# Kernel optimization log

Hardware: AMD Instinct MI355X
Metric: run time of the kernel (lower is better)

## Reference

```python
import jax, jax.numpy as jnp
import numpy as np
from jax import lax

B, T, V, E, H, C, K = 256, 512, 50000, 128, 256, 128, 2


def setup_inputs() -> dict:
    key = jax.random.key(0)
    ks = jax.random.split(key, 16)
    s = lambda *sh: 1.0 / np.sqrt(sh[0])
    return {
        "input_current": jax.random.randint(ks[0], (B, T), 0, V, dtype=jnp.int32),
        "input_left": jax.random.randint(ks[1], (B, T), 0, V, dtype=jnp.int32),
        "input_right": jax.random.randint(ks[2], (B, T), 0, V, dtype=jnp.int32),
        "emb": jax.random.normal(ks[3], (V, E), jnp.float32) * 0.05,
        "Wf": jax.random.normal(ks[4], (E, H), jnp.float32) * s(E),
        "Uf": jax.random.normal(ks[5], (H, H), jnp.float32) * s(H),
        "bf": jnp.zeros((H,), jnp.float32),
        "Wb": jax.random.normal(ks[6], (E, H), jnp.float32) * s(E),
        "Ub": jax.random.normal(ks[7], (H, H), jnp.float32) * s(H),
        "bb": jnp.zeros((H,), jnp.float32),
        "Wc": jax.random.normal(ks[8], (2 * H + E, C), jnp.float32) * s(2 * H + E),
        "bc": jnp.zeros((C,), jnp.float32),
        "Wd": jax.random.normal(ks[9], (C, K), jnp.float32) * s(C),
        "bd": jnp.zeros((K,), jnp.float32),
    }


def _simple_rnn(x, W, U, b):
    # x: [B,T,E] -> outputs [B,T,H]; h_t = tanh(x_t W + b + h_{t-1} U)
    xw = jnp.einsum("bte,eh->bth", x, W) + b  # precompute input projection
    h0 = jnp.zeros((x.shape[0], U.shape[0]), x.dtype)

    def step(h, xw_t):
        h = jnp.tanh(xw_t + h @ U)
        return h, h

    _, hs = lax.scan(step, h0, jnp.swapaxes(xw, 0, 1))  # scan over time
    return jnp.swapaxes(hs, 0, 1)


def reference(input_current, input_left, input_right, emb, Wf, Uf, bf, Wb, Ub, bb, Wc, bc, Wd, bd):
    e_cur = emb[input_current]  # [B,T,E]
    e_left = emb[input_left]
    e_right = emb[input_right]
    x_left = _simple_rnn(e_left, Wf, Uf, bf)  # [B,T,H]
    # go_backwards RNN: process reversed sequence, then model reverses back
    x_right = _simple_rnn(e_right[:, ::-1], Wb, Ub, bb)[:, ::-1]  # [B,T,H]
    x = jnp.concatenate([x_left, e_cur, x_right], axis=2)  # [B,T,2H+E]
    x = jnp.tanh(jnp.einsum("btd,dc->btc", x, Wc) + bc)  # Conv1D k=1 + tanh
    x = jnp.max(x, axis=1)  # GlobalMaxPooling1D
    return jax.nn.sigmoid(x @ Wd + bd)  # [B,K]
```

## Files before the change

### kernel.cpp

```cpp
#include <hip/hip_runtime.h>
#include <hip/hip_bf16.h>


#define B_ 256
#define T_ 512
#define E_ 128
#define H_ 256
#define C_ 128

typedef __attribute__((ext_vector_type(8))) short short8;
typedef __attribute__((ext_vector_type(4))) float float4v;
typedef __attribute__((ext_vector_type(2))) unsigned int uint2v;

__device__ inline unsigned short f2bf(float f) {
  unsigned u = __float_as_uint(f);
  u += 0x7fffu + ((u >> 16) & 1u);
  return (unsigned short)(u >> 16);
}
__device__ inline unsigned pkbf(float a, float b) {
  __hip_bfloat162 h2 = __float22bfloat162_rn(float2{a, b});
  union { __hip_bfloat162 h; unsigned u; } cv;
  cv.h = h2;
  return cv.u;
}
__device__ inline float lo16f(unsigned u) { return __uint_as_float(u << 16); }
__device__ inline float hi16f(unsigned u) { return __uint_as_float(u & 0xffff0000u); }
__device__ inline float fast_tanh(float x) {
  float e = __expf(2.f * x);
  float r = __builtin_amdgcn_rcpf(e + 1.f);
  return __builtin_fmaf(-2.f, r, 1.f);
}
__device__ inline unsigned enc_f(float f) {
  unsigned u = __float_as_uint(f);
  return (u & 0x80000000u) ? ~u : (u | 0x80000000u);
}
__device__ inline float dec_f(unsigned key) {
  unsigned bits = (key & 0x80000000u) ? (key ^ 0x80000000u) : ~key;
  return __uint_as_float(bits);
}
__device__ inline void sync_lds() {
  asm volatile("s_waitcnt lgkmcnt(0)\n\ts_barrier" ::: "memory");
}
__device__ inline int clampt(int t) { return t < 0 ? 0 : (t > 511 ? 511 : t); }

__device__ inline void wait_flag(const int* f) {
  if (__hip_atomic_load(f, __ATOMIC_RELAXED, __HIP_MEMORY_SCOPE_AGENT) == 0) {
    while (__hip_atomic_load(f, __ATOMIC_RELAXED, __HIP_MEMORY_SCOPE_AGENT) ==
           0)
      __builtin_amdgcn_s_sleep(8);
  }
  (void)__hip_atomic_load(f, __ATOMIC_ACQUIRE, __HIP_MEMORY_SCOPE_AGENT);
}

__global__ __launch_bounds__(256) void prep_kernel(
    const float* __restrict__ Wf, const float* __restrict__ Wb,
    const float* __restrict__ Wc, const float* __restrict__ Uf,
    const float* __restrict__ Ub,
    unsigned short* __restrict__ WfT, unsigned short* __restrict__ WbT,
    unsigned short* __restrict__ WcT, unsigned short* __restrict__ UfT,
    unsigned short* __restrict__ UbT, unsigned int* __restrict__ pooled,
    int* __restrict__ flags) {
  int gid = blockIdx.x * 256 + threadIdx.x;
  int stride = gridDim.x * 256;
  for (int i = gid; i < 128 * 256; i += stride) {
    int k = i >> 8, n = i & 255;
    WfT[n * 128 + k] = f2bf(Wf[i]);
    WbT[n * 128 + k] = f2bf(Wb[i]);
  }
  for (int i = gid; i < 640 * 128; i += stride) {
    int k = i >> 7, n = i & 127;
    WcT[n * 640 + k] = f2bf(Wc[i]);
  }
  for (int i = gid; i < 256 * 256; i += stride) {
    int k = i >> 8, n = i & 255;
    UfT[n * 256 + k] = f2bf(Uf[i]);
    UbT[n * 256 + k] = f2bf(Ub[i]);
  }
  for (int i = gid; i < B_ * C_; i += stride) pooled[i] = 0u;
  for (int i = gid; i < 1024; i += stride) flags[i] = 0;
}

__global__ __launch_bounds__(512, 1) void fused_kernel(
    const int* __restrict__ idxL, const int* __restrict__ idxR,
    const int* __restrict__ idxC, const float* __restrict__ emb,
    const unsigned short* __restrict__ WfT,
    const unsigned short* __restrict__ WbT,
    const float* __restrict__ bfv, const float* __restrict__ bbv,
    const unsigned short* __restrict__ UfT,
    const unsigned short* __restrict__ UbT, unsigned short* x,
    int* __restrict__ flags) {
  const int blk = blockIdx.x;
  const int tid = threadIdx.x;
  const int lane = tid & 63, q = lane >> 4, l15 = lane & 15;

  __shared__ __attribute__((aligned(16))) unsigned short hbuf[2][16][280];

  if (blk < 32) {
    const int dir = blk & 1;
    const int btile = blk >> 1;
    const int b0 = btile * 16;
    const unsigned short* __restrict__ UT = dir ? UbT : UfT;
    const int xoff = dir ? 384 : 0;
    const int tstep = dir ? -1 : 1;
    const int t0 = dir ? (T_ - 1) : 0;
    const ptrdiff_t dstep = (ptrdiff_t)tstep * 640;
    const int wv = tid >> 6;
    const int* fl = flags + (dir * 16 + btile) * 32;

    unsigned short* hb0 = &hbuf[0][0][0];
    unsigned short* hb1 = &hbuf[1][0][0];
    for (int i = tid; i < 16 * 280; i += 512) hb0[i] = 0;

    short8 ufr[2][8];
#pragma unroll
    for (int mt = 0; mt < 2; ++mt)
#pragma unroll
      for (int kt = 0; kt < 8; ++kt)
        ufr[mt][kt] = *(const short8*)(UT + (32 * wv + 16 * mt + l15) * H_ +
                                       kt * 32 + q * 8);

    int lastc = dir ? 31 : 0;
    wait_flag(fl + lastc);

    unsigned short* ptrS[2];
    const unsigned short* ptrL[2];
    uint2v curA[2], curB[2], infA[2], infB[2];
#pragma unroll
    for (int mt = 0; mt < 2; ++mt) {
      unsigned short* base =
          x + (size_t)(b0 + 2 * wv + mt) * T_ * 640 + xoff + lane * 4;
      unsigned short* bt = base + (ptrdiff_t)t0 * 640;
      curA[mt] = *(const uint2v*)(bt);
      curB[mt] = *(const uint2v*)(bt + dstep);
      infA[mt] = *(const uint2v*)(bt + 2 * dstep);
      infB[mt] = *(const uint2v*)(bt + 3 * dstep);
      ptrS[mt] = bt;
      ptrL[mt] = bt + 4 * dstep;
    }

    const unsigned lrd = l15 * 280;
    const unsigned lwr = l15 * 280 + 32 * wv;

    __syncthreads();

#pragma unroll 1
    for (int p = 0; p < 256; ++p) {
      int c = dir ? ((506 - 2 * p) >> 4) : ((2 * p + 5) >> 4);
      c = c < 0 ? 0 : (c > 31 ? 31 : c);
      if (c != lastc) {
        wait_flag(fl + c);
        lastc = c;
      }
      uint2v ldA[2], ldB[2];
      if (p < 254) {
#pragma unroll
        for (int mt = 0; mt < 2; ++mt) {
          ldA[mt] = *(const uint2v*)(ptrL[mt]);
          ldB[mt] = *(const uint2v*)(ptrL[mt] + dstep);
        }
      } else {
#pragma unroll
        for (int mt = 0; mt < 2; ++mt) {
          ldA[mt] = infA[mt];
          ldB[mt] = infB[mt];
        }
      }
#pragma unroll
      for (int mt = 0; mt < 2; ++mt) ptrL[mt] += 2 * dstep;

      {
        short8 afr[8];
#pragma unroll
        for (int kt = 0; kt < 8; ++kt)
          afr[kt] = *(const short8*)(hb0 + lrd + kt * 32 + q * 8);
        float4v acc[2];
#pragma unroll
        for (int mt = 0; mt < 2; ++mt)
          acc[mt] = (float4v){lo16f(curA[mt].x), hi16f(curA[mt].x),
                              lo16f(curA[mt].y), hi16f(curA[mt].y)};
#pragma unroll
        for (int kt = 0; kt < 8; ++kt)
#pragma unroll
          for (int mt = 0; mt < 2; ++mt)
            acc[mt] = __builtin_amdgcn_mfma_f32_16x16x32_bf16(
                ufr[mt][kt], afr[kt], acc[mt], 0, 0, 0);
#pragma unroll
        for (int mt = 0; mt < 2; ++mt) {
          uint2v hv = {pkbf(fast_tanh(acc[mt][0]), fast_tanh(acc[mt][1])),
                       pkbf(fast_tanh(acc[mt][2]), fast_tanh(acc[mt][3]))};
          *(uint2v*)(hb1 + lwr + 16 * mt + 4 * q) = hv;
          *(uint2v*)ptrS[mt] = hv;
        }
      }
      sync_lds();

      {
        short8 afr[8];
#pragma unroll
        for (int kt = 0; kt < 8; ++kt)
          afr[kt] = *(const short8*)(hb1 + lrd + kt * 32 + q * 8);
        float4v acc[2];
#pragma unroll
        for (int mt = 0; mt < 2; ++mt)
          acc[mt] = (float4v){lo16f(curB[mt].x), hi16f(curB[mt].x),
                              lo16f(curB[mt].y), hi16f(curB[mt].y)};
#pragma unroll
        for (int kt = 0; kt < 8; ++kt)
#pragma unroll
          for (int mt = 0; mt < 2; ++mt)
            acc[mt] = __builtin_amdgcn_mfma_f32_16x16x32_bf16(
                ufr[mt][kt], afr[kt], acc[mt], 0, 0, 0);
#pragma unroll
        for (int mt = 0; mt < 2; ++mt) {
          uint2v hv = {pkbf(fast_tanh(acc[mt][0]), fast_tanh(acc[mt][1])),
                       pkbf(fast_tanh(acc[mt][2]), fast_tanh(acc[mt][3]))};
          *(uint2v*)(hb0 + lwr + 16 * mt + 4 * q) = hv;
          *(uint2v*)(ptrS[mt] + dstep) = hv;
        }
      }
#pragma unroll
      for (int mt = 0; mt < 2; ++mt) {
        ptrS[mt] += 2 * dstep;
        curA[mt] = infA[mt];
        curB[mt] = infB[mt];
        infA[mt] = ldA[mt];
        infB[mt] = ldB[mt];
      }
      sync_lds();
    }
    return;
  }

  if (blk < 1056) {
    const int b2 = blk - 32;
    const int z = b2 >> 5, r = b2 & 31;
    const int btile = r & 15, dirg = r >> 4;
    const int chunk = dirg ? (31 - z) : z;
    const int w8 = tid >> 6;
    const int g = w8 >> 2, wv = w8 & 3;
    const int t0 = chunk * 16 + g * 8;
    const int b0 = btile * 16;
    const int* __restrict__ idx = dirg ? idxR : idxL;
    const unsigned short* __restrict__ WT = dirg ? WbT : WfT;
    const float* __restrict__ bias = dirg ? bbv : bfv;

    short8 wfr[4][4];
#pragma unroll
    for (int mt = 0; mt < 4; ++mt)
#pragma unroll
      for (int kt = 0; kt < 4; ++kt)
        wfr[mt][kt] = *(const short8*)(WT + (64 * wv + 16 * mt + l15) * 128 +
                                       kt * 32 + q * 8);
    float4v bv[4];
#pragma unroll
    for (int mt = 0; mt < 4; ++mt)
      bv[mt] = *(const float4v*)(bias + 64 * wv + 16 * mt + 4 * q);

    int er[8];
#pragma unroll
    for (int j = 0; j < 8; ++j) er[j] = idx[(b0 + l15) * T_ + t0 + j];

    float4v g0[8];
#pragma unroll
    for (int kt = 0; kt < 4; ++kt) {
      const float* p8 = emb + (size_t)er[0] * E_ + kt * 32 + q * 8;
      g0[2 * kt] = *(const float4v*)p8;
      g0[2 * kt + 1] = *(const float4v*)(p8 + 4);
    }

#pragma unroll 1
    for (int j = 0; j < 8; ++j) {
      float4v gn[8];
      if (j < 7) {
#pragma unroll
        for (int kt = 0; kt < 4; ++kt) {
          const float* p8 = emb + (size_t)er[j + 1] * E_ + kt * 32 + q * 8;
          gn[2 * kt] = *(const float4v*)p8;
          gn[2 * kt + 1] = *(const float4v*)(p8 + 4);
        }
      }
      short8 efr[4];
#pragma unroll
      for (int kt = 0; kt < 4; ++kt) {
        union { unsigned u[4]; short8 s; } cv;
        cv.u[0] = pkbf(g0[2 * kt][0], g0[2 * kt][1]);
        cv.u[1] = pkbf(g0[2 * kt][2], g0[2 * kt][3]);
        cv.u[2] = pkbf(g0[2 * kt + 1][0], g0[2 * kt + 1][1]);
        cv.u[3] = pkbf(g0[2 * kt + 1][2], g0[2 * kt + 1][3]);
        efr[kt] = cv.s;
      }
      float4v acc[4];
#pragma unroll
      for (int mt = 0; mt < 4; ++mt) acc[mt] = (float4v){0.f, 0.f, 0.f, 0.f};
#pragma unroll
      for (int kt = 0; kt < 4; ++kt)
#pragma unroll
        for (int mt = 0; mt < 4; ++mt)
          acc[mt] = __builtin_amdgcn_mfma_f32_16x16x32_bf16(
              wfr[mt][kt], efr[kt], acc[mt], 0, 0, 0);
      const int t = t0 + j;
#pragma unroll
      for (int mt = 0; mt < 4; ++mt) {
        float4v v = acc[mt] + bv[mt];
        uint2v pk = {pkbf(v[0], v[1]), pkbf(v[2], v[3])};
        *(uint2v*)(x + ((size_t)(b0 + 4 * wv + mt) * T_ + t) * 640 +
                   dirg * 384 + lane * 4) = pk;
      }
      if (j < 7) {
#pragma unroll
        for (int kk = 0; kk < 8; ++kk) g0[kk] = gn[kk];
      }
    }
    __syncthreads();
    if (tid == 0) {
      __threadfence();
      __hip_atomic_store(flags + (dirg * 16 + btile) * 32 + chunk, 1,
                         __ATOMIC_RELEASE, __HIP_MEMORY_SCOPE_AGENT);
    }
    return;
  }

  {
    const int b3 = blk - 1056;
    const int btile = b3 & 15, tch = b3 >> 4;
    const int b0 = btile * 16;
    const int w8 = tid >> 6;
    const int tA = tch * 16 + 2 * w8, tB = tA + 1;
    const int erA = idxC[(b0 + l15) * T_ + tA];
    const int erB = idxC[(b0 + l15) * T_ + tB];
    const float* epA = emb + (size_t)erA * E_;
    const float* epB = emb + (size_t)erB * E_;
    float4v ga[8], gb[8];
#pragma unroll
    for (int u = 0; u < 8; ++u) ga[u] = *(const float4v*)(epA + 16 * u + 4 * q);
#pragma unroll
    for (int u = 0; u < 8; ++u) gb[u] = *(const float4v*)(epB + 16 * u + 4 * q);
#pragma unroll
    for (int u = 0; u < 8; ++u) {
      uint2v pk = {pkbf(ga[u][0], ga[u][1]), pkbf(ga[u][2], ga[u][3])};
      int row = b0 + u + 8 * (q >> 1);
      *(uint2v*)(x + ((size_t)row * T_ + tA) * 640 + 256 + 64 * (q & 1) +
                 4 * l15) = pk;
    }
#pragma unroll
    for (int u = 0; u < 8; ++u) {
      uint2v pk = {pkbf(gb[u][0], gb[u][1]), pkbf(gb[u][2], gb[u][3])};
      int row = b0 + u + 8 * (q >> 1);
      *(uint2v*)(x + ((size_t)row * T_ + tB) * 640 + 256 + 64 * (q & 1) +
                 4 * l15) = pk;
    }
  }
}

__global__ __launch_bounds__(256, 2) void convpool_kernel(
    const unsigned short* __restrict__ x, const unsigned short* __restrict__ WcT,
    const float* __restrict__ bc, unsigned int* __restrict__ pooled) {
  const int b0 = (blockIdx.x & 15) * 16;
  const int t0 = (blockIdx.x >> 4) * 16;
  const int tid = threadIdx.x;
  const int w = tid >> 6, lane = tid & 63, q = lane >> 4, l15 = lane & 15;

  __shared__ __attribute__((aligned(16))) unsigned short tile[2][16][648];

  short8 wfr[2][20];
#pragma unroll
  for (int ct = 0; ct < 2; ++ct)
#pragma unroll
    for (int kt = 0; kt < 20; ++kt)
      wfr[ct][kt] = *(const short8*)(WcT +
                                     (size_t)(32 * w + 16 * ct + l15) * 640 +
                                     kt * 32 + q * 8);
  float4v bv[2];
#pragma unroll
  for (int ct = 0; ct < 2; ++ct)
    bv[ct] = *(const float4v*)(bc + 32 * w + 16 * ct + 4 * q);

  float4v mx[2];
  mx[0] = (float4v){-1e30f, -1e30f, -1e30f, -1e30f};
  mx[1] = mx[0];

  const int srow = tid >> 4, ssub = tid & 15;
  {
    const unsigned short* src = x + ((size_t)(b0 + srow) * T_ + t0) * 640;
#pragma unroll
    for (int j = 0; j < 5; ++j)
      *(short8*)&tile[0][srow][ssub * 8 + j * 128] =
          *(const short8*)(src + ssub * 8 + j * 128);
  }
  __syncthreads();

#pragma unroll 1
  for (int j = 0; j < 16; ++j) {
    const int t = t0 + j;
    const int buf = j & 1;
    if (j < 15) {
      const unsigned short* src = x + ((size_t)(b0 + srow) * T_ + t + 1) * 640;
#pragma unroll
      for (int jj = 0; jj < 5; ++jj)
        *(short8*)&tile[buf ^ 1][srow][ssub * 8 + jj * 128] =
            *(const short8*)(src + ssub * 8 + jj * 128);
    }
    float4v acc[2];
    acc[0] = (float4v){0.f, 0.f, 0.f, 0.f};
    acc[1] = (float4v){0.f, 0.f, 0.f, 0.f};
#pragma unroll
    for (int kt = 0; kt < 20; ++kt) {
      int row, so1, so2;
      if (kt < 8) {
        row = 2 * kt + (q >> 1);
        so1 = 64 * (2 * (q & 1)) + 4 * l15;
        so2 = so1 + 64;
      } else if (kt < 12) {
        row = 2 * (kt - 8) + (q >> 1) + 8 * (q & 1);
        so1 = 256 + 4 * l15;
        so2 = 320 + 4 * l15;
      } else {
        row = 2 * (kt - 12) + (q >> 1);
        so1 = 384 + 64 * (2 * (q & 1)) + 4 * l15;
        so2 = so1 + 64;
      }
      union { unsigned u[4]; short8 s; } cv;
      uint2v c1 = *(const uint2v*)&tile[buf][row][so1];
      uint2v c2 = *(const uint2v*)&tile[buf][row][so2];
      cv.u[0] = c1.x; cv.u[1] = c1.y; cv.u[2] = c2.x; cv.u[3] = c2.y;
      acc[0] = __builtin_amdgcn_mfma_f32_16x16x32_bf16(wfr[0][kt], cv.s,
                                                       acc[0], 0, 0, 0);
      acc[1] = __builtin_amdgcn_mfma_f32_16x16x32_bf16(wfr[1][kt], cv.s,
                                                       acc[1], 0, 0, 0);
    }
#pragma unroll
    for (int ct = 0; ct < 2; ++ct)
#pragma unroll
      for (int i = 0; i < 4; ++i)
        mx[ct][i] = fmaxf(mx[ct][i], acc[ct][i]);
    __syncthreads();
  }
#pragma unroll
  for (int ct = 0; ct < 2; ++ct)
#pragma unroll
    for (int i = 0; i < 4; ++i)
      atomicMax(pooled + (b0 + l15) * C_ + 32 * w + 16 * ct + 4 * q + i,
                enc_f(fast_tanh(mx[ct][i] + bv[ct][i])));
}

__global__ __launch_bounds__(256) void dense_kernel(
    const unsigned int* __restrict__ pooled, const float* __restrict__ Wd,
    const float* __restrict__ bd, float* __restrict__ out) {
  int b = threadIdx.x;
  float s0 = bd[0], s1 = bd[1];
#pragma unroll 4
  for (int c = 0; c < C_; ++c) {
    float f = dec_f(pooled[b * C_ + c]);
    s0 += f * Wd[c * 2 + 0];
    s1 += f * Wd[c * 2 + 1];
  }
  out[b * 2 + 0] = 1.f / (1.f + __expf(-s0));
  out[b * 2 + 1] = 1.f / (1.f + __expf(-s1));
}

extern "C" void kernel_launch(void* const* d_in, const int* in_sizes, int n_in,
                              void* d_out, int out_size, void* d_ws, size_t ws_size,
                              hipStream_t stream) {
  const int* idxC = (const int*)d_in[0];
  const int* idxL = (const int*)d_in[1];
  const int* idxR = (const int*)d_in[2];
  const float* emb = (const float*)d_in[3];
  const float* Wf = (const float*)d_in[4];
  const float* Uf = (const float*)d_in[5];
  const float* bf_ = (const float*)d_in[6];
  const float* Wb = (const float*)d_in[7];
  const float* Ub = (const float*)d_in[8];
  const float* bb_ = (const float*)d_in[9];
  const float* Wc = (const float*)d_in[10];
  const float* bc = (const float*)d_in[11];
  const float* Wd = (const float*)d_in[12];
  const float* bd = (const float*)d_in[13];

  char* ws = (char*)d_ws;
  unsigned short* x = (unsigned short*)ws;
  unsigned int* pooled = (unsigned int*)(ws + 167772160);
  unsigned short* WfT = (unsigned short*)(ws + 167903232);
  unsigned short* WbT = WfT + 256 * 128;
  unsigned short* WcT = WbT + 256 * 128;
  unsigned short* UfT = WcT + 128 * 640;
  unsigned short* UbT = UfT + 256 * 256;
  int* flags = (int*)(ws + 168460288);

  prep_kernel<<<64, 256, 0, stream>>>(Wf, Wb, Wc, Uf, Ub, WfT, WbT, WcT, UfT,
                                      UbT, pooled, flags);
  fused_kernel<<<1568, 512, 120 * 1024, stream>>>(idxL, idxR, idxC, emb, WfT,
                                                  WbT, bf_, bb_, UfT, UbT, x,
                                                  flags);
  convpool_kernel<<<512, 256, 0, stream>>>(x, WcT, bc, pooled);
  dense_kernel<<<1, 256, 0, stream>>>(pooled, Wd, bd, (float*)d_out);
}
```

Measured before the change: 592.5 us.

## Fuse conv+maxpool into persistent kernel, overlapping it with the recurrences via flags

```diff
diff --git a/kernel.cpp b/kernel.cpp
--- a/kernel.cpp
+++ b/kernel.cpp
@@ -41,12 +41,11 @@
 __device__ inline void sync_lds() {
   asm volatile("s_waitcnt lgkmcnt(0)\n\ts_barrier" ::: "memory");
 }
-__device__ inline int clampt(int t) { return t < 0 ? 0 : (t > 511 ? 511 : t); }
-
-__device__ inline void wait_flag(const int* f) {
-  if (__hip_atomic_load(f, __ATOMIC_RELAXED, __HIP_MEMORY_SCOPE_AGENT) == 0) {
-    while (__hip_atomic_load(f, __ATOMIC_RELAXED, __HIP_MEMORY_SCOPE_AGENT) ==
-           0)
+
+__device__ inline void wait_flag_ge(const int* f, int v) {
+  if (__hip_atomic_load(f, __ATOMIC_RELAXED, __HIP_MEMORY_SCOPE_AGENT) < v) {
+    while (__hip_atomic_load(f, __ATOMIC_RELAXED, __HIP_MEMORY_SCOPE_AGENT) <
+           v)
       __builtin_amdgcn_s_sleep(8);
   }
   (void)__hip_atomic_load(f, __ATOMIC_ACQUIRE, __HIP_MEMORY_SCOPE_AGENT);
@@ -87,7 +86,9 @@
     const unsigned short* __restrict__ WbT,
     const float* __restrict__ bfv, const float* __restrict__ bbv,
     const unsigned short* __restrict__ UfT,
-    const unsigned short* __restrict__ UbT, unsigned short* x,
+    const unsigned short* __restrict__ UbT,
+    const unsigned short* __restrict__ WcT, const float* __restrict__ bc,
+    unsigned short* x, unsigned int* __restrict__ pooled,
     int* __restrict__ flags) {
   const int blk = blockIdx.x;
   const int tid = threadIdx.x;
@@ -105,7 +106,7 @@
     const int t0 = dir ? (T_ - 1) : 0;
     const ptrdiff_t dstep = (ptrdiff_t)tstep * 640;
     const int wv = tid >> 6;
-    const int* fl = flags + (dir * 16 + btile) * 32;
+    int* fl = flags + (dir * 16 + btile) * 32;
 
     unsigned short* hb0 = &hbuf[0][0][0];
     unsigned short* hb1 = &hbuf[1][0][0];
@@ -120,7 +121,7 @@
                                        kt * 32 + q * 8);
 
     int lastc = dir ? 31 : 0;
-    wait_flag(fl + lastc);
+    wait_flag_ge(fl + lastc, 1);
 
     unsigned short* ptrS[2];
     const unsigned short* ptrL[2];
@@ -148,7 +149,7 @@
       int c = dir ? ((506 - 2 * p) >> 4) : ((2 * p + 5) >> 4);
       c = c < 0 ? 0 : (c > 31 ? 31 : c);
       if (c != lastc) {
-        wait_flag(fl + c);
+        wait_flag_ge(fl + c, 1);
         lastc = c;
       }
       uint2v ldA[2], ldB[2];
@@ -226,7 +227,17 @@
         infA[mt] = ldA[mt];
         infB[mt] = ldB[mt];
       }
-      sync_lds();
+      if (((p + 1) & 7) == 0) {
+        asm volatile("s_waitcnt vmcnt(0) lgkmcnt(0)\n\ts_barrier" ::: "memory");
+        if (tid == 0) {
+          const int cdone = dir ? (32 - ((p + 1) >> 3)) : (((p + 1) >> 3) - 1);
+          __threadfence();
+          __hip_atomic_store(fl + cdone, 2, __ATOMIC_RELEASE,
+                             __HIP_MEMORY_SCOPE_AGENT);
+        }
+      } else {
+        sync_lds();
+      }
     }
     return;
   }
@@ -321,126 +332,106 @@
   }
 
   {
-    const int b3 = blk - 1056;
-    const int btile = b3 & 15, tch = b3 >> 4;
+    extern __shared__ unsigned short dtile[];
+    const int b2 = blk - 1056;
+    const int btile = b2 & 15, g = b2 >> 4;
     const int b0 = btile * 16;
-    const int w8 = tid >> 6;
-    const int tA = tch * 16 + 2 * w8, tB = tA + 1;
-    const int erA = idxC[(b0 + l15) * T_ + tA];
-    const int erB = idxC[(b0 + l15) * T_ + tB];
-    const float* epA = emb + (size_t)erA * E_;
-    const float* epB = emb + (size_t)erB * E_;
-    float4v ga[8], gb[8];
-#pragma unroll
-    for (int u = 0; u < 8; ++u) ga[u] = *(const float4v*)(epA + 16 * u + 4 * q);
-#pragma unroll
-    for (int u = 0; u < 8; ++u) gb[u] = *(const float4v*)(epB + 16 * u + 4 * q);
-#pragma unroll
-    for (int u = 0; u < 8; ++u) {
-      uint2v pk = {pkbf(ga[u][0], ga[u][1]), pkbf(ga[u][2], ga[u][3])};
-      int row = b0 + u + 8 * (q >> 1);
-      *(uint2v*)(x + ((size_t)row * T_ + tA) * 640 + 256 + 64 * (q & 1) +
-                 4 * l15) = pk;
-    }
-#pragma unroll
-    for (int u = 0; u < 8; ++u) {
-      uint2v pk = {pkbf(gb[u][0], gb[u][1]), pkbf(gb[u][2], gb[u][3])};
-      int row = b0 + u + 8 * (q >> 1);
-      *(uint2v*)(x + ((size_t)row * T_ + tB) * 640 + 256 + 64 * (q & 1) +
-                 4 * l15) = pk;
-    }
-  }
-}
-
-__global__ __launch_bounds__(256, 2) void convpool_kernel(
-    const unsigned short* __restrict__ x, const unsigned short* __restrict__ WcT,
-    const float* __restrict__ bc, unsigned int* __restrict__ pooled) {
-  const int b0 = (blockIdx.x & 15) * 16;
-  const int t0 = (blockIdx.x >> 4) * 16;
-  const int tid = threadIdx.x;
-  const int w = tid >> 6, lane = tid & 63, q = lane >> 4, l15 = lane & 15;
-
-  __shared__ __attribute__((aligned(16))) unsigned short tile[2][16][648];
-
-  short8 wfr[2][20];
-#pragma unroll
-  for (int ct = 0; ct < 2; ++ct)
+    const int w = tid >> 6;
+
+    short8 wfr[20];
 #pragma unroll
     for (int kt = 0; kt < 20; ++kt)
-      wfr[ct][kt] = *(const short8*)(WcT +
-                                     (size_t)(32 * w + 16 * ct + l15) * 640 +
-                                     kt * 32 + q * 8);
-  float4v bv[2];
-#pragma unroll
-  for (int ct = 0; ct < 2; ++ct)
-    bv[ct] = *(const float4v*)(bc + 32 * w + 16 * ct + 4 * q);
-
-  float4v mx[2];
-  mx[0] = (float4v){-1e30f, -1e30f, -1e30f, -1e30f};
-  mx[1] = mx[0];
-
-  const int srow = tid >> 4, ssub = tid & 15;
-  {
-    const unsigned short* src = x + ((size_t)(b0 + srow) * T_ + t0) * 640;
-#pragma unroll
-    for (int j = 0; j < 5; ++j)
-      *(short8*)&tile[0][srow][ssub * 8 + j * 128] =
-          *(const short8*)(src + ssub * 8 + j * 128);
-  }
-  __syncthreads();
+      wfr[kt] =
+          *(const short8*)(WcT + (size_t)(16 * w + l15) * 640 + kt * 32 + q * 8);
+    float4v bv = *(const float4v*)(bc + 16 * w + 4 * q);
+
+    float4v mx = (float4v){-1e30f, -1e30f, -1e30f, -1e30f};
+
+    const int* flF = flags + btile * 32;
+    const int* flB = flags + (16 + btile) * 32;
+
+    const int srow = tid >> 4;
+    const int tt0 = srow >> 4, row0 = srow & 15;
+    const int ssub = tid & 15;
+    const int f0 = 16 * (row0 & 7) + 8 * (row0 >> 3);
 
 #pragma unroll 1
-  for (int j = 0; j < 16; ++j) {
-    const int t = t0 + j;
-    const int buf = j & 1;
-    if (j < 15) {
-      const unsigned short* src = x + ((size_t)(b0 + srow) * T_ + t + 1) * 640;
-#pragma unroll
-      for (int jj = 0; jj < 5; ++jj)
-        *(short8*)&tile[buf ^ 1][srow][ssub * 8 + jj * 128] =
-            *(const short8*)(src + ssub * 8 + jj * 128);
-    }
-    float4v acc[2];
-    acc[0] = (float4v){0.f, 0.f, 0.f, 0.f};
-    acc[1] = (float4v){0.f, 0.f, 0.f, 0.f};
-#pragma unroll
-    for (int kt = 0; kt < 20; ++kt) {
-      int row, so1, so2;
-      if (kt < 8) {
-        row = 2 * kt + (q >> 1);
-        so1 = 64 * (2 * (q & 1)) + 4 * l15;
-        so2 = so1 + 64;
-      } else if (kt < 12) {
-        row = 2 * (kt - 8) + (q >> 1) + 8 * (q & 1);
-        so1 = 256 + 4 * l15;
-        so2 = 320 + 4 * l15;
-      } else {
-        row = 2 * (kt - 12) + (q >> 1);
-        so1 = 384 + 64 * (2 * (q & 1)) + 4 * l15;
-        so2 = so1 + 64;
-      }
-      union { unsigned u[4]; short8 s; } cv;
-      uint2v c1 = *(const uint2v*)&tile[buf][row][so1];
-      uint2v c2 = *(const uint2v*)&tile[buf][row][so2];
-      cv.u[0] = c1.x; cv.u[1] = c1.y; cv.u[2] = c2.x; cv.u[3] = c2.y;
-      acc[0] = __builtin_amdgcn_mfma_f32_16x16x32_bf16(wfr[0][kt], cv.s,
-                                                       acc[0], 0, 0, 0);
-      acc[1] = __builtin_amdgcn_mfma_f32_16x16x32_bf16(wfr[1][kt], cv.s,
-                                                       acc[1], 0, 0, 0);
-    }
-#pragma unroll
-    for (int ct = 0; ct < 2; ++ct)
-#pragma unroll
-      for (int i = 0; i < 4; ++i)
-        mx[ct][i] = fmaxf(mx[ct][i], acc[ct][i]);
-    __syncthreads();
-  }
-#pragma unroll
-  for (int ct = 0; ct < 2; ++ct)
+    for (int s = 0; s < 4; ++s) {
+      const int rk = g + 8 * s;
+      const int c = (rk & 1) ? (16 + (rk >> 1)) : (15 - (rk >> 1));
+      wait_flag_ge(flF + c, 2);
+      wait_flag_ge(flB + c, 2);
+      const int t0c = c * 16;
+
+      auto stage = [&](int jp, int buf) {
+        const int t = t0c + 2 * jp + tt0;
+        const unsigned short* src = x + ((size_t)(b0 + row0) * T_ + t) * 640;
+        unsigned short* dst =
+            dtile + (size_t)((buf * 2 + tt0) * 16 + row0) * 648;
+        *(short8*)(dst + ssub * 8) = *(const short8*)(src + ssub * 8);
+        *(short8*)(dst + 128 + ssub * 8) = *(const short8*)(src + 128 + ssub * 8);
+        *(short8*)(dst + 384 + ssub * 8) = *(const short8*)(src + 384 + ssub * 8);
+        *(short8*)(dst + 512 + ssub * 8) = *(const short8*)(src + 512 + ssub * 8);
+        const int er = idxC[(b0 + ssub) * T_ + t];
+        const float* ep = emb + (size_t)er * E_ + f0;
+        float4v e0 = *(const float4v*)ep;
+        float4v e1 = *(const float4v*)(ep + 4);
+        *(uint2v*)(dst + 256 + 4 * ssub) =
+            (uint2v){pkbf(e0[0], e0[1]), pkbf(e0[2], e0[3])};
+        *(uint2v*)(dst + 320 + 4 * ssub) =
+            (uint2v){pkbf(e1[0], e1[1]), pkbf(e1[2], e1[3])};
+      };
+
+      stage(0, 0);
+      __syncthreads();
+#pragma unroll 1
+      for (int jp = 0; jp < 8; ++jp) {
+        const int buf = jp & 1;
+        if (jp < 7) stage(jp + 1, buf ^ 1);
+        float4v acc0 = (float4v){0.f, 0.f, 0.f, 0.f};
+        float4v acc1 = acc0;
+#pragma unroll
+        for (int kt = 0; kt < 20; ++kt) {
+          int rrow, so1, so2;
+          if (kt < 8) {
+            rrow = 2 * kt + (q >> 1);
+            so1 = 128 * (q & 1) + 4 * l15;
+            so2 = so1 + 64;
+          } else if (kt < 12) {
+            rrow = 2 * (kt - 8) + (q >> 1) + 8 * (q & 1);
+            so1 = 256 + 4 * l15;
+            so2 = 320 + 4 * l15;
+          } else {
+            rrow = 2 * (kt - 12) + (q >> 1);
+            so1 = 384 + 128 * (q & 1) + 4 * l15;
+            so2 = so1 + 64;
+          }
+          const unsigned short* r0p =
+              dtile + (size_t)((buf * 2) * 16 + rrow) * 648;
+          const unsigned short* r1p = r0p + 16 * 648;
+          uint2v a1 = *(const uint2v*)(r0p + so1);
+          uint2v a2 = *(const uint2v*)(r0p + so2);
+          uint2v b1 = *(const uint2v*)(r1p + so1);
+          uint2v b2 = *(const uint2v*)(r1p + so2);
+          union { unsigned u[4]; short8 s8; } cva, cvb;
+          cva.u[0] = a1.x; cva.u[1] = a1.y; cva.u[2] = a2.x; cva.u[3] = a2.y;
+          cvb.u[0] = b1.x; cvb.u[1] = b1.y; cvb.u[2] = b2.x; cvb.u[3] = b2.y;
+          acc0 = __builtin_amdgcn_mfma_f32_16x16x32_bf16(wfr[kt], cva.s8,
+                                                         acc0, 0, 0, 0);
+          acc1 = __builtin_amdgcn_mfma_f32_16x16x32_bf16(wfr[kt], cvb.s8,
+                                                         acc1, 0, 0, 0);
+        }
+#pragma unroll
+        for (int i = 0; i < 4; ++i)
+          mx[i] = fmaxf(fmaxf(mx[i], acc0[i]), acc1[i]);
+        __syncthreads();
+      }
+    }
 #pragma unroll
     for (int i = 0; i < 4; ++i)
-      atomicMax(pooled + (b0 + l15) * C_ + 32 * w + 16 * ct + 4 * q + i,
-                enc_f(fast_tanh(mx[ct][i] + bv[ct][i])));
+      atomicMax(pooled + (b0 + l15) * C_ + 16 * w + 4 * q + i,
+                enc_f(fast_tanh(mx[i] + bv[i])));
+  }
 }
 
 __global__ __launch_bounds__(256) void dense_kernel(
@@ -488,9 +479,8 @@
 
   prep_kernel<<<64, 256, 0, stream>>>(Wf, Wb, Wc, Uf, Ub, WfT, WbT, WcT, UfT,
                                       UbT, pooled, flags);
-  fused_kernel<<<1568, 512, 120 * 1024, stream>>>(idxL, idxR, idxC, emb, WfT,
-                                                  WbT, bf_, bb_, UfT, UbT, x,
-                                                  flags);
-  convpool_kernel<<<512, 256, 0, stream>>>(x, WcT, bc, pooled);
+  fused_kernel<<<1184, 512, 120 * 1024, stream>>>(idxL, idxR, idxC, emb, WfT,
+                                                  WbT, bf_, bb_, UfT, UbT, WcT,
+                                                  bc, x, pooled, flags);
   dense_kernel<<<1, 256, 0, stream>>>(pooled, Wd, bd, (float*)d_out);
 }
```

Result: slower. 627.6 us (+5.9%).
